# Performance work log

Hardware: AMD Instinct MI355X
Metric: run time of the kernel (lower is better)

Reference implementation:

```python
import jax, jax.numpy as jnp
import numpy as np
from math import sqrt

B, S, E, H = 2, 2048, 1024, 16

def setup_inputs() -> dict:
    key = jax.random.key(0)
    k1, k2, k3, k4, k5 = jax.random.split(key, 5)
    bound_in = 1.0 / sqrt(E)
    return {
        "inputs": jax.random.normal(k1, (B, S, E), dtype=jnp.float32),
        "W_in": jax.random.uniform(k2, (3 * E, E), dtype=jnp.float32, minval=-bound_in, maxval=bound_in),
        "b_in": jax.random.uniform(k3, (3 * E,), dtype=jnp.float32, minval=-bound_in, maxval=bound_in),
        "W_out": jax.random.uniform(k4, (E, E), dtype=jnp.float32, minval=-bound_in, maxval=bound_in),
        "b_out": jax.random.uniform(k5, (E,), dtype=jnp.float32, minval=-bound_in, maxval=bound_in),
    }

def reference(inputs, W_in, b_in, W_out, b_out):
    # Eval-mode forward (dropout is identity when not training).
    b, s, e = inputs.shape
    hd = e // H
    qkv = jnp.einsum('bse,fe->bsf', inputs, W_in) + b_in  # [B,S,3E]
    q, k, v = jnp.split(qkv, 3, axis=-1)
    # [B,S,E] -> [B,H,S,hd]
    to_heads = lambda t: t.reshape(b, s, H, hd).transpose(0, 2, 1, 3)
    q, k, v = to_heads(q), to_heads(k), to_heads(v)
    scores = jnp.einsum('bhqd,bhkd->bhqk', q, k) / jnp.sqrt(jnp.float32(hd))
    causal = jnp.tril(jnp.ones((s, s), dtype=bool))
    scores = jnp.where(causal, scores, -jnp.inf)
    attn = jax.nn.softmax(scores, axis=-1)  # stable max-subtract softmax, same math
    out = jnp.einsum('bhqk,bhkd->bhqd', attn, v)  # [B,H,S,hd]
    out = out.transpose(0, 2, 1, 3).reshape(b, s, e)
    return jnp.einsum('bse,fe->bsf', out, W_out) + b_out
```

## Files before the change

kernel.cpp:

```cpp
#include <hip/hip_runtime.h>
#include <hip/hip_bf16.h>
#include <stdint.h>

#define SS 2048
#define EE 1024
#define HH 16
#define HD 64

#define QSCALE 0.1803368801111137f

typedef __attribute__((ext_vector_type(8))) short short8;
typedef __attribute__((ext_vector_type(4))) float f32x4;

__device__ __forceinline__ short f2bf(float f) {
  union { float f; uint32_t u; } x; x.f = f;
  uint32_t r = x.u + 0x7fffu + ((x.u >> 16) & 1u);
  return (short)(r >> 16);
}

__device__ __forceinline__ uint32_t pk_bf16(float a, float b) {
#if __has_builtin(__builtin_amdgcn_cvt_pk_bf16_f32)
  typedef __attribute__((ext_vector_type(2))) __bf16 bf16x2_t;
  union { bf16x2_t v; uint32_t u; } x;
  x.v = __builtin_amdgcn_cvt_pk_bf16_f32(a, b);
  return x.u;
#else
  return (uint32_t)(uint16_t)f2bf(a) | ((uint32_t)(uint16_t)f2bf(b) << 16);
#endif
}

#if __has_builtin(__builtin_amdgcn_exp2f)
#define EXP2F __builtin_amdgcn_exp2f
#else
#define EXP2F exp2f
#endif

__device__ __forceinline__ void async_cp16(const void* g, void* l) {
  __builtin_amdgcn_global_load_lds((const __attribute__((address_space(1))) void*)g,
                                   (__attribute__((address_space(3))) void*)l, 16, 0, 0);
}

#define N4_X  1048576
#define N4_W1 786432
#define N4_W2 262144
__global__ __launch_bounds__(256) void cvt_all(
    const float* __restrict__ x, const float* __restrict__ w1,
    const float* __restrict__ w2,
    short* __restrict__ xb, short* __restrict__ w1b, short* __restrict__ w2b)
{
  int i = blockIdx.x * 256 + threadIdx.x;
  const float* src; short* dst; int off;
  if (i < N4_X)            { src = x;  dst = xb;  off = i; }
  else if (i < N4_X+N4_W1) { src = w1; dst = w1b; off = i - N4_X; }
  else                     { src = w2; dst = w2b; off = i - N4_X - N4_W1; }
  float4 v = *(const float4*)&src[(size_t)off * 4];
  uint2 pk;
  pk.x = pk_bf16(v.x, v.y);
  pk.y = pk_bf16(v.z, v.w);
  *(uint2*)&dst[(size_t)off * 4] = pk;
}

__global__ __launch_bounds__(256) void gemm_qkv(
    const short* __restrict__ A, const short* __restrict__ Bw,
    const float* __restrict__ bias,
    short* __restrict__ qw, short* __restrict__ kw, short* __restrict__ vw,
    int M, int N, int K)
{
  __shared__ short smem[17408];
  const int tid = threadIdx.x;
  const int lane = tid & 63;
  const int wv = tid >> 6;
  const int wm = (wv >> 1) * 64;
  const int wn = (wv & 1) * 64;
  const int t = lane >> 4;
  const int lr = lane & 15;
  const int bm = blockIdx.y * 128;
  const int bn = blockIdx.x * 128;

  f32x4 acc[4][4];
  #pragma unroll
  for (int i = 0; i < 4; ++i)
    #pragma unroll
    for (int j = 0; j < 4; ++j) acc[i][j] = (f32x4){0.f, 0.f, 0.f, 0.f};

  auto stage = [&](int buf, int k0) {
    short* sA = smem + buf * 8192;
    short* sB = smem + buf * 8192 + 4096;
    #pragma unroll
    for (int it = 0; it < 2; ++it) {
      int c = it * 256 + wv * 64 + lane;
      int row = c >> 2;
      int ch = (c & 3) * 8;
      async_cp16(&A[(size_t)(bm + row) * K + k0 + ch],
                 (char*)sA + (size_t)(it * 256 + wv * 64) * 16);
      async_cp16(&Bw[(size_t)(bn + row) * K + k0 + ch],
                 (char*)sB + (size_t)(it * 256 + wv * 64) * 16);
    }
  };

  const bool isV = (bn >= 2048);
  const bool isQ = (bn < 1024);
  const int nk = K >> 5;
  stage(0, 0);
  __syncthreads();

  if (isV) {
    for (int k = 0; k < nk; ++k) {
      if (k + 1 < nk) stage((k + 1) & 1, (k + 1) << 5);
      const short* cA = smem + (k & 1) * 8192;
      const short* cB = smem + (k & 1) * 8192 + 4096;
      short8 af[4], bfr[4];
      #pragma unroll
      for (int i = 0; i < 4; ++i) af[i] = *(const short8*)&cA[(wm + i*16 + lr)*32 + t*8];
      #pragma unroll
      for (int j = 0; j < 4; ++j) bfr[j] = *(const short8*)&cB[(wn + j*16 + lr)*32 + t*8];
      #pragma unroll
      for (int i = 0; i < 4; ++i)
        #pragma unroll
        for (int j = 0; j < 4; ++j)
          acc[i][j] = __builtin_amdgcn_mfma_f32_16x16x32_bf16(af[i], bfr[j], acc[i][j], 0, 0, 0);
      __syncthreads();
    }
  } else {
    for (int k = 0; k < nk; ++k) {
      if (k + 1 < nk) stage((k + 1) & 1, (k + 1) << 5);
      const short* cA = smem + (k & 1) * 8192;
      const short* cB = smem + (k & 1) * 8192 + 4096;
      short8 af[4], bfr[4];
      #pragma unroll
      for (int i = 0; i < 4; ++i) af[i] = *(const short8*)&cA[(wm + i*16 + lr)*32 + t*8];
      #pragma unroll
      for (int j = 0; j < 4; ++j) bfr[j] = *(const short8*)&cB[(wn + j*16 + lr)*32 + t*8];
      #pragma unroll
      for (int i = 0; i < 4; ++i)
        #pragma unroll
        for (int j = 0; j < 4; ++j)
          acc[i][j] = __builtin_amdgcn_mfma_f32_16x16x32_bf16(bfr[j], af[i], acc[i][j], 0, 0, 0);
      __syncthreads();
    }
  }

  short* vx = smem;
  int b_ = bm >> 11;
  int s0 = bm & 2047;
  if (isV) {
    #pragma unroll
    for (int i = 0; i < 4; ++i) {
      int row0 = wm + i*16 + t*4;
      #pragma unroll
      for (int j = 0; j < 4; ++j) {
        int cl = wn + j*16 + lr;
        float bv = bias[bn + cl];
        uint2 pw;
        pw.x = pk_bf16(acc[i][j][0] + bv, acc[i][j][1] + bv);
        pw.y = pk_bf16(acc[i][j][2] + bv, acc[i][j][3] + bv);
        *(uint2*)&vx[cl*136 + row0] = pw;
      }
    }
    __syncthreads();
    int h0 = (bn - 2048) >> 6;
    #pragma unroll
    for (int it = 0; it < 8; ++it) {
      int cc = it * 256 + tid;
      int cl = cc >> 4;
      int ck = cc & 15;
      int h = h0 + (cl >> 6);
      int d = cl & 63;
      int f = ck >> 2, tt = ck & 3;
      const short* src = &vx[cl*136 + 32*f + 4*tt];
      uint2 lo = *(const uint2*)src;
      uint2 hi = *(const uint2*)(src + 16);
      uint4 val; val.x = lo.x; val.y = lo.y; val.z = hi.x; val.w = hi.y;
      *(uint4*)&vw[((size_t)(b_*HH + h)*HD + d)*SS + s0 + ck*8] = val;
    }
  } else {
    #pragma unroll
    for (int j = 0; j < 4; ++j) {
      int col0 = wn + j*16 + t*4;
      float4 bv4 = *(const float4*)&bias[bn + col0];
      #pragma unroll
      for (int i = 0; i < 4; ++i) {
        int row = wm + i*16 + lr;
        float v0 = acc[i][j][0] + bv4.x;
        float v1 = acc[i][j][1] + bv4.y;
        float v2 = acc[i][j][2] + bv4.z;
        float v3 = acc[i][j][3] + bv4.w;
        if (isQ) { v0 *= QSCALE; v1 *= QSCALE; v2 *= QSCALE; v3 *= QSCALE; }
        uint2 pw;
        pw.x = pk_bf16(v0, v1);
        pw.y = pk_bf16(v2, v3);
        *(uint2*)&vx[row*136 + col0] = pw;
      }
    }
    __syncthreads();
    short* dst = isQ ? qw : kw;
    int h0 = (bn & 1023) >> 6;
    #pragma unroll
    for (int it = 0; it < 8; ++it) {
      int cc = it * 256 + tid;
      int row = cc >> 4;
      int ck = cc & 15;
      int h = h0 + (ck >> 3);
      int d0 = (ck & 7) * 8;
      *(uint4*)&dst[((size_t)(b_*HH + h)*SS + s0 + row)*HD + d0] =
          *(const uint4*)&vx[row*136 + ck*8];
    }
  }
}

__global__ __launch_bounds__(256) void gemm_out(
    const short* __restrict__ A, const short* __restrict__ Bw,
    const float* __restrict__ bias,
    float* __restrict__ C,
    int M, int N, int K)
{
  __shared__ short smem[12288];
  const int tid = threadIdx.x;
  const int lane = tid & 63;
  const int wv = tid >> 6;
  const int wm = (wv >> 1) * 32;
  const int wn = (wv & 1) * 64;
  const int t = lane >> 4;
  const int lr = lane & 15;
  const int bm = blockIdx.y * 64;
  const int bn = blockIdx.x * 128;

  f32x4 acc[2][4];
  #pragma unroll
  for (int i = 0; i < 2; ++i)
    #pragma unroll
    for (int j = 0; j < 4; ++j) acc[i][j] = (f32x4){0.f, 0.f, 0.f, 0.f};

  auto stage = [&](int buf, int k0) {
    short* sA = smem + buf * 6144;
    short* sB = smem + buf * 6144 + 2048;
    {
      int c = wv * 64 + lane;
      int row = c >> 2;
      int ch = (c & 3) * 8;
      async_cp16(&A[(size_t)(bm + row) * K + k0 + ch],
                 (char*)sA + (size_t)(wv * 64) * 16);
    }
    #pragma unroll
    for (int it = 0; it < 2; ++it) {
      int c = it * 256 + wv * 64 + lane;
      int row = c >> 2;
      int ch = (c & 3) * 8;
      async_cp16(&Bw[(size_t)(bn + row) * K + k0 + ch],
                 (char*)sB + (size_t)(it * 256 + wv * 64) * 16);
    }
  };

  const int nk = K >> 5;
  stage(0, 0);
  __syncthreads();

  for (int k = 0; k < nk; ++k) {
    if (k + 1 < nk) stage((k + 1) & 1, (k + 1) << 5);
    const short* cA = smem + (k & 1) * 6144;
    const short* cB = smem + (k & 1) * 6144 + 2048;
    short8 af[2], bfr[4];
    #pragma unroll
    for (int i = 0; i < 2; ++i) af[i] = *(const short8*)&cA[(wm + i*16 + lr)*32 + t*8];
    #pragma unroll
    for (int j = 0; j < 4; ++j) bfr[j] = *(const short8*)&cB[(wn + j*16 + lr)*32 + t*8];
    #pragma unroll
    for (int i = 0; i < 2; ++i)
      #pragma unroll
      for (int j = 0; j < 4; ++j)
        acc[i][j] = __builtin_amdgcn_mfma_f32_16x16x32_bf16(af[i], bfr[j], acc[i][j], 0, 0, 0);
    __syncthreads();
  }

  #pragma unroll
  for (int i = 0; i < 2; ++i) {
    int row0 = bm + wm + i*16 + t*4;
    #pragma unroll
    for (int j = 0; j < 4; ++j) {
      int col = bn + wn + j*16 + lr;
      float bv = bias[col];
      #pragma unroll
      for (int r = 0; r < 4; ++r)
        C[(size_t)(row0 + r) * N + col] = acc[i][j][r] + bv;
    }
  }
}

template<int MODE, typename TA>
__global__ __launch_bounds__(256) void gemm_bt(
    const TA* __restrict__ A, const float* __restrict__ Bw,
    const float* __restrict__ bias,
    float* __restrict__ C,
    short* __restrict__ qw, short* __restrict__ kw, short* __restrict__ vw,
    int M, int N, int K)
{
  __shared__ short sA[128*32];
  __shared__ short sB[128*32];
  const int tid = threadIdx.x;
  const int lane = tid & 63;
  const int wv = tid >> 6;
  const int wm = (wv >> 1) * 64;
  const int wn = (wv & 1) * 64;
  const int t = lane >> 4;
  const int lr = lane & 15;
  const int bm = blockIdx.y * 128;
  const int bn = blockIdx.x * 128;

  f32x4 acc[4][4];
  #pragma unroll
  for (int i = 0; i < 4; ++i)
    #pragma unroll
    for (int j = 0; j < 4; ++j) acc[i][j] = (f32x4){0.f, 0.f, 0.f, 0.f};

  for (int k0 = 0; k0 < K; k0 += 32) {
    __syncthreads();
    if constexpr (sizeof(TA) == 4) {
      #pragma unroll
      for (int it = 0; it < 4; ++it) {
        int c = it * 256 + tid;
        int row = c >> 3, ch = (c & 7) * 4;
        float4 va = *(const float4*)&A[(size_t)(bm + row)*K + k0 + ch];
        uint2 pk; pk.x = pk_bf16(va.x, va.y); pk.y = pk_bf16(va.z, va.w);
        *(uint2*)&sA[row*32 + ch] = pk;
      }
    } else {
      #pragma unroll
      for (int it = 0; it < 2; ++it) {
        int c = it * 256 + tid;
        int row = c >> 2, ch = (c & 3) * 8;
        *(uint4*)&sA[row*32 + ch] = *(const uint4*)&A[(size_t)(bm + row)*K + k0 + ch];
      }
    }
    #pragma unroll
    for (int it = 0; it < 4; ++it) {
      int c = it * 256 + tid;
      int row = c >> 3, ch = (c & 7) * 4;
      float4 vb = *(const float4*)&Bw[(size_t)(bn + row)*K + k0 + ch];
      uint2 pk; pk.x = pk_bf16(vb.x, vb.y); pk.y = pk_bf16(vb.z, vb.w);
      *(uint2*)&sB[row*32 + ch] = pk;
    }
    __syncthreads();
    short8 af[4], bfr[4];
    #pragma unroll
    for (int i = 0; i < 4; ++i) af[i] = *(const short8*)&sA[(wm + i*16 + lr)*32 + t*8];
    #pragma unroll
    for (int j = 0; j < 4; ++j) bfr[j] = *(const short8*)&sB[(wn + j*16 + lr)*32 + t*8];
    #pragma unroll
    for (int i = 0; i < 4; ++i)
      #pragma unroll
      for (int j = 0; j < 4; ++j)
        acc[i][j] = __builtin_amdgcn_mfma_f32_16x16x32_bf16(af[i], bfr[j], acc[i][j], 0, 0, 0);
  }

  #pragma unroll
  for (int i = 0; i < 4; ++i) {
    int row0 = bm + wm + i*16 + t*4;
    #pragma unroll
    for (int j = 0; j < 4; ++j) {
      int col = bn + wn + j*16 + lr;
      float bv = bias[col];
      #pragma unroll
      for (int r = 0; r < 4; ++r) {
        float v = acc[i][j][r] + bv;
        int rr = row0 + r;
        if (MODE == 0) {
          C[(size_t)rr * N + col] = v;
        } else {
          int which = col >> 10;
          int e = col & 1023;
          int h = e >> 6, d = e & 63;
          int b_ = rr >> 11, s = rr & 2047;
          if (which == 0)
            qw[((size_t)(b_*HH + h)*SS + s)*HD + d] = f2bf(v * QSCALE);
          else if (which == 1)
            kw[((size_t)(b_*HH + h)*SS + s)*HD + d] = f2bf(v);
          else {
            int k7 = s & 127;
            int sp = (k7 & 0x60) | ((k7 & 0x0C) << 1) | ((k7 & 0x10) >> 2) | (k7 & 3);
            vw[((size_t)(b_*HH + h)*HD + d)*SS + (s & ~127) + sp] = f2bf(v);
          }
        }
      }
    }
  }
}

__global__ __launch_bounds__(512) void attn_kernel(
    const short* __restrict__ Q, const short* __restrict__ K,
    const short* __restrict__ Vt, short* __restrict__ O)
{
  __shared__ short sK[2][128*64];
  __shared__ short sV[2][64*128];
  const int tid = threadIdx.x;
  const int lane = tid & 63;
  const int w = tid >> 6;
  const int t = lane >> 4;
  const int lr = lane & 15;
  const int blk = blockIdx.x;
  const int qt = (blk < 256) ? (blk >> 5) : (15 - ((blk - 256) >> 5));
  const int bh = blk & 31;
  const int b = bh >> 4, h = bh & 15;
  const short* Qb = Q  + (size_t)bh * SS * HD;
  const short* Kb = K  + (size_t)bh * SS * HD;
  const short* Vb = Vt + (size_t)bh * HD * SS;
  const int qrow0 = qt * 128 + w * 16;

  auto stage = [&](int buf, int kb) {
    #pragma unroll
    for (int it2 = 0; it2 < 2; ++it2) {
      int s = it2 * 512 + tid;
      int krow = s >> 3;
      int kcc = (s & 7) ^ (krow & 7);
      async_cp16(&Kb[(size_t)(kb + krow) * HD + kcc * 8],
                 (char*)sK[buf] + (size_t)(it2 * 512 + w * 64) * 16);
      int d = s >> 4;
      int vcc = (s & 15) ^ (d & 15);
      async_cp16(&Vb[(size_t)d * SS + kb + vcc * 8],
                 (char*)sV[buf] + (size_t)(it2 * 512 + w * 64) * 16);
    }
  };

  short8 qf[2];
  #pragma unroll
  for (int st = 0; st < 2; ++st)
    qf[st] = *(const short8*)&Qb[(size_t)(qrow0 + lr) * HD + st*32 + t*8];

  f32x4 o[4];
  #pragma unroll
  for (int jd = 0; jd < 4; ++jd) o[jd] = (f32x4){0.f, 0.f, 0.f, 0.f};
  float l = 0.f;

  const int niter = qt + 1;
  stage(0, 0);
  __syncthreads();
  int cur = 0;

  #pragma unroll 1
  for (int it = 0; it < niter; ++it) {
    const int kb = it * 128;
    if (it + 1 < niter) stage(cur ^ 1, kb + 128);
    const short* sKc = sK[cur];
    const short* sVc = sV[cur];

    f32x4 sc[8];
    #pragma unroll
    for (int c = 0; c < 8; ++c) sc[c] = (f32x4){0.f,0.f,0.f,0.f};
    __builtin_amdgcn_s_setprio(1);
    #pragma unroll
    for (int c = 0; c < 8; ++c) {
      int krow = c*16 + lr;
      #pragma unroll
      for (int st = 0; st < 2; ++st) {
        int slot = krow*8 + ((st*4 + t) ^ (lr & 7));
        short8 kf = *(const short8*)&sKc[slot*8];
        sc[c] = __builtin_amdgcn_mfma_f32_16x16x32_bf16(kf, qf[st], sc[c], 0, 0, 0);
      }
    }
    __builtin_amdgcn_s_setprio(0);

    if (it == niter - 1) {
      int qg = qrow0 + lr;
      #pragma unroll
      for (int c = 0; c < 8; ++c)
        #pragma unroll
        for (int r = 0; r < 4; ++r)
          if (kb + c*16 + t*4 + r > qg) sc[c][r] = -1e30f;
    }

    float rs0 = 0.f, rs1 = 0.f, rs2 = 0.f, rs3 = 0.f;
    #pragma unroll
    for (int c = 0; c < 8; ++c) {
      sc[c][0] = EXP2F(sc[c][0]);
      sc[c][1] = EXP2F(sc[c][1]);
      sc[c][2] = EXP2F(sc[c][2]);
      sc[c][3] = EXP2F(sc[c][3]);
      rs0 += sc[c][0];
      rs1 += sc[c][1];
      rs2 += sc[c][2];
      rs3 += sc[c][3];
    }
    float rs = (rs0 + rs1) + (rs2 + rs3);
    rs += __shfl_xor(rs, 16);
    rs += __shfl_xor(rs, 32);
    l += rs;

    __builtin_amdgcn_s_setprio(1);
    #pragma unroll
    for (int f = 0; f < 4; ++f) {
      union { uint32_t u[4]; short8 s8; } up;
      up.u[0] = pk_bf16(sc[2*f  ][0], sc[2*f  ][1]);
      up.u[1] = pk_bf16(sc[2*f  ][2], sc[2*f  ][3]);
      up.u[2] = pk_bf16(sc[2*f+1][0], sc[2*f+1][1]);
      up.u[3] = pk_bf16(sc[2*f+1][2], sc[2*f+1][3]);
      short8 pf = up.s8;
      #pragma unroll
      for (int jd = 0; jd < 4; ++jd) {
        int d = jd*16 + lr;
        int vslot = d*16 + ((f*4 + t) ^ lr);
        short8 vf = *(const short8*)&sVc[vslot*8];
        o[jd] = __builtin_amdgcn_mfma_f32_16x16x32_bf16(vf, pf, o[jd], 0, 0, 0);
      }
    }
    __builtin_amdgcn_s_setprio(0);

    __syncthreads();
    cur ^= 1;
  }

  float linv = 1.0f / l;
  size_t rowoff = ((size_t)(b * SS + qrow0 + lr)) * EE + h * HD;
  #pragma unroll
  for (int jd = 0; jd < 4; ++jd) {
    uint2 pw;
    pw.x = pk_bf16(o[jd][0] * linv, o[jd][1] * linv);
    pw.y = pk_bf16(o[jd][2] * linv, o[jd][3] * linv);
    *(uint2*)&O[rowoff + jd*16 + t*4] = pw;
  }
}

extern "C" void kernel_launch(void* const* d_in, const int* in_sizes, int n_in,
                              void* d_out, int out_size, void* d_ws, size_t ws_size,
                              hipStream_t stream) {
  const float* X     = (const float*)d_in[0];
  const float* W_in  = (const float*)d_in[1];
  const float* b_in  = (const float*)d_in[2];
  const float* W_out = (const float*)d_in[3];
  const float* b_out = (const float*)d_in[4];
  float* out = (float*)d_out;

  char* ws = (char*)d_ws;
  const size_t MB = 1024 * 1024;
  const int M = 2 * SS;

  if (ws_size >= 48 * MB) {
    short* Xb   = (short*)(ws);
    short* Wb1  = (short*)(ws + 8  * MB);
    short* Wb2  = (short*)(ws + 14 * MB);
    short* q_ws = (short*)(ws + 16 * MB);
    short* k_ws = (short*)(ws + 24 * MB);
    short* v_ws = (short*)(ws + 32 * MB);
    short* attn = (short*)(ws + 40 * MB);

    cvt_all<<<8192, 256, 0, stream>>>(X, W_in, W_out, Xb, Wb1, Wb2);
    gemm_qkv<<<dim3(24, 32), 256, 0, stream>>>(
        Xb, Wb1, b_in, q_ws, k_ws, v_ws, M, 3 * EE, EE);
    attn_kernel<<<dim3(512), 512, 0, stream>>>(q_ws, k_ws, v_ws, attn);
    gemm_out<<<dim3(8, 64), 256, 0, stream>>>(
        attn, Wb2, b_out, out, M, EE, EE);
  } else {
    short* q_ws = (short*)(ws);
    short* k_ws = (short*)(ws + 8  * MB);
    short* v_ws = (short*)(ws + 16 * MB);
    short* attn = (short*)(ws + 24 * MB);

    gemm_bt<1, float><<<dim3(24, 32), 256, 0, stream>>>(
        X, W_in, b_in, nullptr, q_ws, k_ws, v_ws, M, 3 * EE, EE);
    attn_kernel<<<dim3(512), 512, 0, stream>>>(q_ws, k_ws, v_ws, attn);
    gemm_bt<0, short><<<dim3(8, 32), 256, 0, stream>>>(
        attn, W_out, b_out, out, nullptr, nullptr, nullptr, M, EE, EE);
  }
}
```

Measured before the change: 178.2 us.

## Triple-buffer GEMM async loads with vmcnt waits; enlarge out-proj tile

```diff
diff --git a/kernel.cpp b/kernel.cpp
--- a/kernel.cpp
+++ b/kernel.cpp
@@ -39,6 +39,19 @@
   __builtin_amdgcn_global_load_lds((const __attribute__((address_space(1))) void*)g,
                                    (__attribute__((address_space(3))) void*)l, 16, 0, 0);
 }
+
+#define WAIT_LGKM0_VMCNT4_BARRIER() do {                         \
+    asm volatile("s_waitcnt lgkmcnt(0)" ::: "memory");           \
+    asm volatile("s_waitcnt vmcnt(4)" ::: "memory");             \
+    __builtin_amdgcn_sched_barrier(0);                           \
+    __builtin_amdgcn_s_barrier();                                \
+  } while (0)
+
+#define WAIT_VM0_BARRIER() do {                                  \
+    asm volatile("s_waitcnt vmcnt(0)" ::: "memory");             \
+    __builtin_amdgcn_sched_barrier(0);                           \
+    __builtin_amdgcn_s_barrier();                                \
+  } while (0)
 
 #define N4_X  1048576
 #define N4_W1 786432
@@ -66,7 +79,7 @@
     short* __restrict__ qw, short* __restrict__ kw, short* __restrict__ vw,
     int M, int N, int K)
 {
-  __shared__ short smem[17408];
+  __shared__ short smem[24576];
   const int tid = threadIdx.x;
   const int lane = tid & 63;
   const int wv = tid >> 6;
@@ -85,7 +98,7 @@
 
   auto stage = [&](int buf, int k0) {
     short* sA = smem + buf * 8192;
-    short* sB = smem + buf * 8192 + 4096;
+    short* sB = sA + 4096;
     #pragma unroll
     for (int it = 0; it < 2; ++it) {
       int c = it * 256 + wv * 64 + lane;
@@ -101,14 +114,20 @@
   const bool isV = (bn >= 2048);
   const bool isQ = (bn < 1024);
   const int nk = K >> 5;
+
   stage(0, 0);
-  __syncthreads();
+  stage(1, 32);
+  asm volatile("s_waitcnt vmcnt(4)" ::: "memory");
+  __builtin_amdgcn_sched_barrier(0);
+  __builtin_amdgcn_s_barrier();
 
   if (isV) {
+    #pragma unroll 1
     for (int k = 0; k < nk; ++k) {
-      if (k + 1 < nk) stage((k + 1) & 1, (k + 1) << 5);
-      const short* cA = smem + (k & 1) * 8192;
-      const short* cB = smem + (k & 1) * 8192 + 4096;
+      int k2 = (k + 2 < nk) ? (k + 2) : (nk - 1);
+      stage((k + 2) % 3, k2 << 5);
+      const short* cA = smem + (k % 3) * 8192;
+      const short* cB = cA + 4096;
       short8 af[4], bfr[4];
       #pragma unroll
       for (int i = 0; i < 4; ++i) af[i] = *(const short8*)&cA[(wm + i*16 + lr)*32 + t*8];
@@ -119,13 +138,15 @@
         #pragma unroll
         for (int j = 0; j < 4; ++j)
           acc[i][j] = __builtin_amdgcn_mfma_f32_16x16x32_bf16(af[i], bfr[j], acc[i][j], 0, 0, 0);
-      __syncthreads();
+      WAIT_LGKM0_VMCNT4_BARRIER();
     }
   } else {
+    #pragma unroll 1
     for (int k = 0; k < nk; ++k) {
-      if (k + 1 < nk) stage((k + 1) & 1, (k + 1) << 5);
-      const short* cA = smem + (k & 1) * 8192;
-      const short* cB = smem + (k & 1) * 8192 + 4096;
+      int k2 = (k + 2 < nk) ? (k + 2) : (nk - 1);
+      stage((k + 2) % 3, k2 << 5);
+      const short* cA = smem + (k % 3) * 8192;
+      const short* cB = cA + 4096;
       short8 af[4], bfr[4];
       #pragma unroll
       for (int i = 0; i < 4; ++i) af[i] = *(const short8*)&cA[(wm + i*16 + lr)*32 + t*8];
@@ -136,9 +157,11 @@
         #pragma unroll
         for (int j = 0; j < 4; ++j)
           acc[i][j] = __builtin_amdgcn_mfma_f32_16x16x32_bf16(bfr[j], af[i], acc[i][j], 0, 0, 0);
-      __syncthreads();
-    }
-  }
+      WAIT_LGKM0_VMCNT4_BARRIER();
+    }
+  }
+
+  WAIT_VM0_BARRIER();
 
   short* vx = smem;
   int b_ = bm >> 11;
@@ -214,66 +237,69 @@
     float* __restrict__ C,
     int M, int N, int K)
 {
-  __shared__ short smem[12288];
+  __shared__ short smem[24576];
   const int tid = threadIdx.x;
   const int lane = tid & 63;
   const int wv = tid >> 6;
-  const int wm = (wv >> 1) * 32;
+  const int wm = (wv >> 1) * 64;
   const int wn = (wv & 1) * 64;
   const int t = lane >> 4;
   const int lr = lane & 15;
-  const int bm = blockIdx.y * 64;
+  const int bm = blockIdx.y * 128;
   const int bn = blockIdx.x * 128;
 
-  f32x4 acc[2][4];
-  #pragma unroll
-  for (int i = 0; i < 2; ++i)
+  f32x4 acc[4][4];
+  #pragma unroll
+  for (int i = 0; i < 4; ++i)
     #pragma unroll
     for (int j = 0; j < 4; ++j) acc[i][j] = (f32x4){0.f, 0.f, 0.f, 0.f};
 
   auto stage = [&](int buf, int k0) {
-    short* sA = smem + buf * 6144;
-    short* sB = smem + buf * 6144 + 2048;
-    {
-      int c = wv * 64 + lane;
-      int row = c >> 2;
-      int ch = (c & 3) * 8;
-      async_cp16(&A[(size_t)(bm + row) * K + k0 + ch],
-                 (char*)sA + (size_t)(wv * 64) * 16);
-    }
+    short* sA = smem + buf * 8192;
+    short* sB = sA + 4096;
     #pragma unroll
     for (int it = 0; it < 2; ++it) {
       int c = it * 256 + wv * 64 + lane;
       int row = c >> 2;
       int ch = (c & 3) * 8;
+      async_cp16(&A[(size_t)(bm + row) * K + k0 + ch],
+                 (char*)sA + (size_t)(it * 256 + wv * 64) * 16);
       async_cp16(&Bw[(size_t)(bn + row) * K + k0 + ch],
                  (char*)sB + (size_t)(it * 256 + wv * 64) * 16);
     }
   };
 
   const int nk = K >> 5;
+
   stage(0, 0);
-  __syncthreads();
-
+  stage(1, 32);
+  asm volatile("s_waitcnt vmcnt(4)" ::: "memory");
+  __builtin_amdgcn_sched_barrier(0);
+  __builtin_amdgcn_s_barrier();
+
+  #pragma unroll 1
   for (int k = 0; k < nk; ++k) {
-    if (k + 1 < nk) stage((k + 1) & 1, (k + 1) << 5);
-    const short* cA = smem + (k & 1) * 6144;
-    const short* cB = smem + (k & 1) * 6144 + 2048;
-    short8 af[2], bfr[4];
-    #pragma unroll
-    for (int i = 0; i < 2; ++i) af[i] = *(const short8*)&cA[(wm + i*16 + lr)*32 + t*8];
+    int k2 = (k + 2 < nk) ? (k + 2) : (nk - 1);
+    stage((k + 2) % 3, k2 << 5);
+    const short* cA = smem + (k % 3) * 8192;
+    const short* cB = cA + 4096;
+    short8 af[4], bfr[4];
+    #pragma unroll
+    for (int i = 0; i < 4; ++i) af[i] = *(const short8*)&cA[(wm + i*16 + lr)*32 + t*8];
     #pragma unroll
     for (int j = 0; j < 4; ++j) bfr[j] = *(const short8*)&cB[(wn + j*16 + lr)*32 + t*8];
     #pragma unroll
-    for (int i = 0; i < 2; ++i)
+    for (int i = 0; i < 4; ++i)
       #pragma unroll
       for (int j = 0; j < 4; ++j)
         acc[i][j] = __builtin_amdgcn_mfma_f32_16x16x32_bf16(af[i], bfr[j], acc[i][j], 0, 0, 0);
-    __syncthreads();
-  }
-
-  #pragma unroll
-  for (int i = 0; i < 2; ++i) {
+    WAIT_LGKM0_VMCNT4_BARRIER();
+  }
+
+  asm volatile("s_waitcnt vmcnt(0)" ::: "memory");
+
+  #pragma unroll
+  for (int i = 0; i < 4; ++i) {
     int row0 = bm + wm + i*16 + t*4;
     #pragma unroll
     for (int j = 0; j < 4; ++j) {
@@ -545,7 +571,7 @@
     gemm_qkv<<<dim3(24, 32), 256, 0, stream>>>(
         Xb, Wb1, b_in, q_ws, k_ws, v_ws, M, 3 * EE, EE);
     attn_kernel<<<dim3(512), 512, 0, stream>>>(q_ws, k_ws, v_ws, attn);
-    gemm_out<<<dim3(8, 64), 256, 0, stream>>>(
+    gemm_out<<<dim3(8, 32), 256, 0, stream>>>(
         attn, Wb2, b_out, out, M, EE, EE);
   } else {
     short* q_ws = (short*)(ws);
```

Result: slower. 183.0 us (+2.7%).

## Process two 16-row query tiles per wave to reuse K/V fragments

Applied to the files above, without the earlier changes.

```diff
diff --git a/kernel.cpp b/kernel.cpp
--- a/kernel.cpp
+++ b/kernel.cpp
@@ -385,7 +385,7 @@
   }
 }
 
-__global__ __launch_bounds__(512) void attn_kernel(
+__global__ __launch_bounds__(256) void attn_kernel(
     const short* __restrict__ Q, const short* __restrict__ K,
     const short* __restrict__ Vt, short* __restrict__ O)
 {
@@ -403,32 +403,37 @@
   const short* Qb = Q  + (size_t)bh * SS * HD;
   const short* Kb = K  + (size_t)bh * SS * HD;
   const short* Vb = Vt + (size_t)bh * HD * SS;
-  const int qrow0 = qt * 128 + w * 16;
+  const int qrow0 = qt * 128 + w * 32;
 
   auto stage = [&](int buf, int kb) {
     #pragma unroll
-    for (int it2 = 0; it2 < 2; ++it2) {
-      int s = it2 * 512 + tid;
+    for (int it2 = 0; it2 < 4; ++it2) {
+      int s = it2 * 256 + tid;
       int krow = s >> 3;
       int kcc = (s & 7) ^ (krow & 7);
       async_cp16(&Kb[(size_t)(kb + krow) * HD + kcc * 8],
-                 (char*)sK[buf] + (size_t)(it2 * 512 + w * 64) * 16);
+                 (char*)sK[buf] + (size_t)(it2 * 256 + w * 64) * 16);
       int d = s >> 4;
       int vcc = (s & 15) ^ (d & 15);
       async_cp16(&Vb[(size_t)d * SS + kb + vcc * 8],
-                 (char*)sV[buf] + (size_t)(it2 * 512 + w * 64) * 16);
+                 (char*)sV[buf] + (size_t)(it2 * 256 + w * 64) * 16);
     }
   };
 
-  short8 qf[2];
-  #pragma unroll
-  for (int st = 0; st < 2; ++st)
-    qf[st] = *(const short8*)&Qb[(size_t)(qrow0 + lr) * HD + st*32 + t*8];
-
-  f32x4 o[4];
-  #pragma unroll
-  for (int jd = 0; jd < 4; ++jd) o[jd] = (f32x4){0.f, 0.f, 0.f, 0.f};
-  float l = 0.f;
+  short8 qfa[2], qfb[2];
+  #pragma unroll
+  for (int st = 0; st < 2; ++st) {
+    qfa[st] = *(const short8*)&Qb[(size_t)(qrow0 + lr) * HD + st*32 + t*8];
+    qfb[st] = *(const short8*)&Qb[(size_t)(qrow0 + 16 + lr) * HD + st*32 + t*8];
+  }
+
+  f32x4 oa[4], ob[4];
+  #pragma unroll
+  for (int jd = 0; jd < 4; ++jd) {
+    oa[jd] = (f32x4){0.f, 0.f, 0.f, 0.f};
+    ob[jd] = (f32x4){0.f, 0.f, 0.f, 0.f};
+  }
+  float la = 0.f, lb = 0.f;
 
   const int niter = qt + 1;
   stage(0, 0);
@@ -442,9 +447,12 @@
     const short* sKc = sK[cur];
     const short* sVc = sV[cur];
 
-    f32x4 sc[8];
-    #pragma unroll
-    for (int c = 0; c < 8; ++c) sc[c] = (f32x4){0.f,0.f,0.f,0.f};
+    f32x4 sa[8], sb[8];
+    #pragma unroll
+    for (int c = 0; c < 8; ++c) {
+      sa[c] = (f32x4){0.f,0.f,0.f,0.f};
+      sb[c] = (f32x4){0.f,0.f,0.f,0.f};
+    }
     __builtin_amdgcn_s_setprio(1);
     #pragma unroll
     for (int c = 0; c < 8; ++c) {
@@ -453,52 +461,70 @@
       for (int st = 0; st < 2; ++st) {
         int slot = krow*8 + ((st*4 + t) ^ (lr & 7));
         short8 kf = *(const short8*)&sKc[slot*8];
-        sc[c] = __builtin_amdgcn_mfma_f32_16x16x32_bf16(kf, qf[st], sc[c], 0, 0, 0);
+        sa[c] = __builtin_amdgcn_mfma_f32_16x16x32_bf16(kf, qfa[st], sa[c], 0, 0, 0);
+        sb[c] = __builtin_amdgcn_mfma_f32_16x16x32_bf16(kf, qfb[st], sb[c], 0, 0, 0);
       }
     }
     __builtin_amdgcn_s_setprio(0);
 
     if (it == niter - 1) {
-      int qg = qrow0 + lr;
+      int qga = qrow0 + lr;
+      int qgb = qrow0 + 16 + lr;
       #pragma unroll
       for (int c = 0; c < 8; ++c)
         #pragma unroll
-        for (int r = 0; r < 4; ++r)
-          if (kb + c*16 + t*4 + r > qg) sc[c][r] = -1e30f;
-    }
-
-    float rs0 = 0.f, rs1 = 0.f, rs2 = 0.f, rs3 = 0.f;
+        for (int r = 0; r < 4; ++r) {
+          int pos = kb + c*16 + t*4 + r;
+          if (pos > qga) sa[c][r] = -1e30f;
+          if (pos > qgb) sb[c][r] = -1e30f;
+        }
+    }
+
+    float ra0 = 0.f, ra1 = 0.f, rb0 = 0.f, rb1 = 0.f;
     #pragma unroll
     for (int c = 0; c < 8; ++c) {
-      sc[c][0] = EXP2F(sc[c][0]);
-      sc[c][1] = EXP2F(sc[c][1]);
-      sc[c][2] = EXP2F(sc[c][2]);
-      sc[c][3] = EXP2F(sc[c][3]);
-      rs0 += sc[c][0];
-      rs1 += sc[c][1];
-      rs2 += sc[c][2];
-      rs3 += sc[c][3];
-    }
-    float rs = (rs0 + rs1) + (rs2 + rs3);
-    rs += __shfl_xor(rs, 16);
-    rs += __shfl_xor(rs, 32);
-    l += rs;
+      sa[c][0] = EXP2F(sa[c][0]);
+      sa[c][1] = EXP2F(sa[c][1]);
+      sa[c][2] = EXP2F(sa[c][2]);
+      sa[c][3] = EXP2F(sa[c][3]);
+      ra0 += sa[c][0] + sa[c][1];
+      ra1 += sa[c][2] + sa[c][3];
+      sb[c][0] = EXP2F(sb[c][0]);
+      sb[c][1] = EXP2F(sb[c][1]);
+      sb[c][2] = EXP2F(sb[c][2]);
+      sb[c][3] = EXP2F(sb[c][3]);
+      rb0 += sb[c][0] + sb[c][1];
+      rb1 += sb[c][2] + sb[c][3];
+    }
+    float rsa = ra0 + ra1;
+    rsa += __shfl_xor(rsa, 16);
+    rsa += __shfl_xor(rsa, 32);
+    la += rsa;
+    float rsb = rb0 + rb1;
+    rsb += __shfl_xor(rsb, 16);
+    rsb += __shfl_xor(rsb, 32);
+    lb += rsb;
 
     __builtin_amdgcn_s_setprio(1);
     #pragma unroll
     for (int f = 0; f < 4; ++f) {
-      union { uint32_t u[4]; short8 s8; } up;
-      up.u[0] = pk_bf16(sc[2*f  ][0], sc[2*f  ][1]);
-      up.u[1] = pk_bf16(sc[2*f  ][2], sc[2*f  ][3]);
-      up.u[2] = pk_bf16(sc[2*f+1][0], sc[2*f+1][1]);
-      up.u[3] = pk_bf16(sc[2*f+1][2], sc[2*f+1][3]);
-      short8 pf = up.s8;
+      union { uint32_t u[4]; short8 s8; } ua, ub;
+      ua.u[0] = pk_bf16(sa[2*f  ][0], sa[2*f  ][1]);
+      ua.u[1] = pk_bf16(sa[2*f  ][2], sa[2*f  ][3]);
+      ua.u[2] = pk_bf16(sa[2*f+1][0], sa[2*f+1][1]);
+      ua.u[3] = pk_bf16(sa[2*f+1][2], sa[2*f+1][3]);
+      ub.u[0] = pk_bf16(sb[2*f  ][0], sb[2*f  ][1]);
+      ub.u[1] = pk_bf16(sb[2*f  ][2], sb[2*f  ][3]);
+      ub.u[2] = pk_bf16(sb[2*f+1][0], sb[2*f+1][1]);
+      ub.u[3] = pk_bf16(sb[2*f+1][2], sb[2*f+1][3]);
+      short8 pfa = ua.s8, pfb = ub.s8;
       #pragma unroll
       for (int jd = 0; jd < 4; ++jd) {
         int d = jd*16 + lr;
         int vslot = d*16 + ((f*4 + t) ^ lr);
         short8 vf = *(const short8*)&sVc[vslot*8];
-        o[jd] = __builtin_amdgcn_mfma_f32_16x16x32_bf16(vf, pf, o[jd], 0, 0, 0);
+        oa[jd] = __builtin_amdgcn_mfma_f32_16x16x32_bf16(vf, pfa, oa[jd], 0, 0, 0);
+        ob[jd] = __builtin_amdgcn_mfma_f32_16x16x32_bf16(vf, pfb, ob[jd], 0, 0, 0);
       }
     }
     __builtin_amdgcn_s_setprio(0);
@@ -507,14 +533,19 @@
     cur ^= 1;
   }
 
-  float linv = 1.0f / l;
-  size_t rowoff = ((size_t)(b * SS + qrow0 + lr)) * EE + h * HD;
+  float lia = 1.0f / la;
+  float lib = 1.0f / lb;
+  size_t rowa = ((size_t)(b * SS + qrow0 + lr)) * EE + h * HD;
+  size_t rowb = ((size_t)(b * SS + qrow0 + 16 + lr)) * EE + h * HD;
   #pragma unroll
   for (int jd = 0; jd < 4; ++jd) {
-    uint2 pw;
-    pw.x = pk_bf16(o[jd][0] * linv, o[jd][1] * linv);
-    pw.y = pk_bf16(o[jd][2] * linv, o[jd][3] * linv);
-    *(uint2*)&O[rowoff + jd*16 + t*4] = pw;
+    uint2 pa, pb;
+    pa.x = pk_bf16(oa[jd][0] * lia, oa[jd][1] * lia);
+    pa.y = pk_bf16(oa[jd][2] * lia, oa[jd][3] * lia);
+    *(uint2*)&O[rowa + jd*16 + t*4] = pa;
+    pb.x = pk_bf16(ob[jd][0] * lib, ob[jd][1] * lib);
+    pb.y = pk_bf16(ob[jd][2] * lib, ob[jd][3] * lib);
+    *(uint2*)&O[rowb + jd*16 + t*4] = pb;
   }
 }
 
@@ -544,7 +575,7 @@
     cvt_all<<<8192, 256, 0, stream>>>(X, W_in, W_out, Xb, Wb1, Wb2);
     gemm_qkv<<<dim3(24, 32), 256, 0, stream>>>(
         Xb, Wb1, b_in, q_ws, k_ws, v_ws, M, 3 * EE, EE);
-    attn_kernel<<<dim3(512), 512, 0, stream>>>(q_ws, k_ws, v_ws, attn);
+    attn_kernel<<<dim3(512), 256, 0, stream>>>(q_ws, k_ws, v_ws, attn);
     gemm_out<<<dim3(8, 64), 256, 0, stream>>>(
         attn, Wb2, b_out, out, M, EE, EE);
   } else {
@@ -555,7 +586,7 @@
 
     gemm_bt<1, float><<<dim3(24, 32), 256, 0, stream>>>(
         X, W_in, b_in, nullptr, q_ws, k_ws, v_ws, M, 3 * EE, EE);
-    attn_kernel<<<dim3(512), 512, 0, stream>>>(q_ws, k_ws, v_ws, attn);
+    attn_kernel<<<dim3(512), 256, 0, stream>>>(q_ws, k_ws, v_ws, attn);
     gemm_bt<0, short><<<dim3(8, 32), 256, 0, stream>>>(
         attn, W_out, b_out, out, nullptr, nullptr, nullptr, M, EE, EE);
   }
```

New measurement: 183.0 us. 1.03x slower.

## Peel diagonal attention tile to skip masked chunks; grid-stride cvt kernel

Applied to the files above, without the earlier changes.

```diff
diff --git a/kernel.cpp b/kernel.cpp
--- a/kernel.cpp
+++ b/kernel.cpp
@@ -43,21 +43,23 @@
 #define N4_X  1048576
 #define N4_W1 786432
 #define N4_W2 262144
+#define N4_ALL (N4_X + N4_W1 + N4_W2)
 __global__ __launch_bounds__(256) void cvt_all(
     const float* __restrict__ x, const float* __restrict__ w1,
     const float* __restrict__ w2,
     short* __restrict__ xb, short* __restrict__ w1b, short* __restrict__ w2b)
 {
-  int i = blockIdx.x * 256 + threadIdx.x;
-  const float* src; short* dst; int off;
-  if (i < N4_X)            { src = x;  dst = xb;  off = i; }
-  else if (i < N4_X+N4_W1) { src = w1; dst = w1b; off = i - N4_X; }
-  else                     { src = w2; dst = w2b; off = i - N4_X - N4_W1; }
-  float4 v = *(const float4*)&src[(size_t)off * 4];
-  uint2 pk;
-  pk.x = pk_bf16(v.x, v.y);
-  pk.y = pk_bf16(v.z, v.w);
-  *(uint2*)&dst[(size_t)off * 4] = pk;
+  for (int i = blockIdx.x * 256 + threadIdx.x; i < N4_ALL; i += 2048 * 256) {
+    const float* src; short* dst; int off;
+    if (i < N4_X)            { src = x;  dst = xb;  off = i; }
+    else if (i < N4_X+N4_W1) { src = w1; dst = w1b; off = i - N4_X; }
+    else                     { src = w2; dst = w2b; off = i - N4_X - N4_W1; }
+    float4 v = *(const float4*)&src[(size_t)off * 4];
+    uint2 pk;
+    pk.x = pk_bf16(v.x, v.y);
+    pk.y = pk_bf16(v.z, v.w);
+    *(uint2*)&dst[(size_t)off * 4] = pk;
+  }
 }
 
 __global__ __launch_bounds__(256) void gemm_qkv(
@@ -436,9 +438,9 @@
   int cur = 0;
 
   #pragma unroll 1
-  for (int it = 0; it < niter; ++it) {
+  for (int it = 0; it < niter - 1; ++it) {
     const int kb = it * 128;
-    if (it + 1 < niter) stage(cur ^ 1, kb + 128);
+    stage(cur ^ 1, kb + 128);
     const short* sKc = sK[cur];
     const short* sVc = sV[cur];
 
@@ -457,15 +459,6 @@
       }
     }
     __builtin_amdgcn_s_setprio(0);
-
-    if (it == niter - 1) {
-      int qg = qrow0 + lr;
-      #pragma unroll
-      for (int c = 0; c < 8; ++c)
-        #pragma unroll
-        for (int r = 0; r < 4; ++r)
-          if (kb + c*16 + t*4 + r > qg) sc[c][r] = -1e30f;
-    }
 
     float rs0 = 0.f, rs1 = 0.f, rs2 = 0.f, rs3 = 0.f;
     #pragma unroll
@@ -507,6 +500,74 @@
     cur ^= 1;
   }
 
+  {
+    const short* sKc = sK[cur];
+    const short* sVc = sV[cur];
+
+    f32x4 sc[8];
+    #pragma unroll
+    for (int c = 0; c < 8; ++c) sc[c] = (f32x4){0.f,0.f,0.f,0.f};
+    __builtin_amdgcn_s_setprio(1);
+    #pragma unroll
+    for (int c = 0; c < 8; ++c) {
+      if (c > w) continue;
+      int krow = c*16 + lr;
+      #pragma unroll
+      for (int st = 0; st < 2; ++st) {
+        int slot = krow*8 + ((st*4 + t) ^ (lr & 7));
+        short8 kf = *(const short8*)&sKc[slot*8];
+        sc[c] = __builtin_amdgcn_mfma_f32_16x16x32_bf16(kf, qf[st], sc[c], 0, 0, 0);
+      }
+    }
+    __builtin_amdgcn_s_setprio(0);
+
+    #pragma unroll
+    for (int c = 0; c < 8; ++c) {
+      if (c != w) continue;
+      #pragma unroll
+      for (int r = 0; r < 4; ++r)
+        if (4*t + r > lr) sc[c][r] = -1e30f;
+    }
+
+    float rs0 = 0.f, rs1 = 0.f, rs2 = 0.f, rs3 = 0.f;
+    #pragma unroll
+    for (int c = 0; c < 8; ++c) {
+      if (c > w) continue;
+      sc[c][0] = EXP2F(sc[c][0]);
+      sc[c][1] = EXP2F(sc[c][1]);
+      sc[c][2] = EXP2F(sc[c][2]);
+      sc[c][3] = EXP2F(sc[c][3]);
+      rs0 += sc[c][0];
+      rs1 += sc[c][1];
+      rs2 += sc[c][2];
+      rs3 += sc[c][3];
+    }
+    float rs = (rs0 + rs1) + (rs2 + rs3);
+    rs += __shfl_xor(rs, 16);
+    rs += __shfl_xor(rs, 32);
+    l += rs;
+
+    __builtin_amdgcn_s_setprio(1);
+    #pragma unroll
+    for (int f = 0; f < 4; ++f) {
+      if (f > (w >> 1)) continue;
+      union { uint32_t u[4]; short8 s8; } up;
+      up.u[0] = pk_bf16(sc[2*f  ][0], sc[2*f  ][1]);
+      up.u[1] = pk_bf16(sc[2*f  ][2], sc[2*f  ][3]);
+      up.u[2] = pk_bf16(sc[2*f+1][0], sc[2*f+1][1]);
+      up.u[3] = pk_bf16(sc[2*f+1][2], sc[2*f+1][3]);
+      short8 pf = up.s8;
+      #pragma unroll
+      for (int jd = 0; jd < 4; ++jd) {
+        int d = jd*16 + lr;
+        int vslot = d*16 + ((f*4 + t) ^ lr);
+        short8 vf = *(const short8*)&sVc[vslot*8];
+        o[jd] = __builtin_amdgcn_mfma_f32_16x16x32_bf16(vf, pf, o[jd], 0, 0, 0);
+      }
+    }
+    __builtin_amdgcn_s_setprio(0);
+  }
+
   float linv = 1.0f / l;
   size_t rowoff = ((size_t)(b * SS + qrow0 + lr)) * EE + h * HD;
   #pragma unroll
@@ -541,7 +602,7 @@
     short* v_ws = (short*)(ws + 32 * MB);
     short* attn = (short*)(ws + 40 * MB);
 
-    cvt_all<<<8192, 256, 0, stream>>>(X, W_in, W_out, Xb, Wb1, Wb2);
+    cvt_all<<<2048, 256, 0, stream>>>(X, W_in, W_out, Xb, Wb1, Wb2);
     gemm_qkv<<<dim3(24, 32), 256, 0, stream>>>(
         Xb, Wb1, b_in, q_ws, k_ws, v_ws, M, 3 * EE, EE);
     attn_kernel<<<dim3(512), 512, 0, stream>>>(q_ws, k_ws, v_ws, attn);
```

New measurement: 182.3 us. 2.3% more time.
